# Optimization experiments

Hardware: AMD Instinct MI355X
Metric: run time of the kernel (lower is better)

## Reference

```python
import jax, jax.numpy as jnp
import numpy as np

N_TOK, D_MODEL, D_INT, N_EXP, TOP_K = 16384, 1024, 512, 8, 2


def setup_inputs() -> dict:
    key = jax.random.key(0)
    k1, k2, k3, k4 = jax.random.split(key, 4)
    x = jax.random.normal(k1, (N_TOK, D_MODEL), jnp.float32)
    # gate projection weight (n_experts, d_model)
    wg = jax.random.normal(k2, (N_EXP, D_MODEL), jnp.float32) * 0.02
    # fc1: (n_experts, 2*d_intermediate, d_model); fc2: (n_experts, d_model, d_intermediate)
    fc1 = jax.random.normal(k3, (N_EXP, 2 * D_INT, D_MODEL), jnp.float32) * (1.0 / np.sqrt(D_MODEL))
    fc2 = jax.random.normal(k4, (N_EXP, D_MODEL, D_INT), jnp.float32) * (1.0 / np.sqrt(D_INT))
    return {"x": x, "wg": wg, "fc1": fc1, "fc2": fc2, "top_k": TOP_K}


def reference(x, wg, fc1, fc2, top_k):
    # --- Gate: softmax scores, top-k selection, renormalized combine weights ---
    scores = jax.nn.softmax(x @ wg.T, axis=-1)            # (n_tok, n_exp)
    w, idx = jax.lax.top_k(scores, top_k)                 # (n_tok, k)
    w = w / jnp.sum(w, axis=-1, keepdims=True)
    # --- Routed experts: gated MLP per expert, weighted combine ---
    # Equivalent math to sort-by-expert dispatch + grouped GEMM + scatter combine:
    # each token's output = sum_k w_k * f_{idx_k}(x). We loop over the small fixed
    # expert set and mask, avoiding a (n_tok, n_exp, 2*d_int) intermediate.
    n_exp = fc1.shape[0]
    out = jnp.zeros_like(x)
    for e in range(n_exp):
        coef = jnp.sum(jnp.where(idx == e, w, 0.0), axis=-1)  # (n_tok,)
        h = x @ fc1[e].T                                      # (n_tok, 2*d_int)
        y, g = jnp.split(h, 2, axis=-1)
        y = (y * jax.nn.silu(g)) @ fc2[e].T                   # (n_tok, d_model)
        out = out + coef[:, None] * y
    return out
```

## Files before the change

### kernel.cpp

```cpp
#include <hip/hip_runtime.h>
#include <hip/hip_bf16.h>
#include <cstdint>


#define NT 16384
#define DM 1024
#define DI 512
#define NE 8
#define NB 16
#define HB 64
#define MT1 128

typedef __attribute__((ext_vector_type(8))) short bf16x8;
typedef __attribute__((ext_vector_type(4))) float f32x4;

__device__ __forceinline__ void gl16(const void* g, void* l) {
  __builtin_amdgcn_global_load_lds(
      (const __attribute__((address_space(1))) void*)g,
      (__attribute__((address_space(3))) void*)l, 16, 0, 0);
}

__device__ __forceinline__ ushort f2bf(float f) {
  uint32_t x = __float_as_uint(f);
  return (ushort)((x + 0x7fffu + ((x >> 16) & 1u)) >> 16);
}

__global__ __launch_bounds__(256) void f2bf_kernel(const float* __restrict__ in,
                                                   ushort* __restrict__ out, int n8) {
  int i = blockIdx.x * 256 + threadIdx.x;
  if (i >= n8) return;
  const float4* p = (const float4*)(in + (size_t)i * 8);
  float4 a = p[0], b = p[1];
  union { ushort u[8]; int4 v; } o;
  o.u[0] = f2bf(a.x); o.u[1] = f2bf(a.y); o.u[2] = f2bf(a.z); o.u[3] = f2bf(a.w);
  o.u[4] = f2bf(b.x); o.u[5] = f2bf(b.y); o.u[6] = f2bf(b.z); o.u[7] = f2bf(b.w);
  *(int4*)(out + (size_t)i * 8) = o.v;
}

__global__ __launch_bounds__(256) void gate_kernel(
    const float* __restrict__ x, const float* __restrict__ wg,
    int* __restrict__ topk_idx, float* __restrict__ topk_w,
    ushort* __restrict__ xb) {
  __shared__ float wgs[NE * DM];
  for (int i = threadIdx.x; i < NE * DM; i += 256) wgs[i] = wg[i];
  __syncthreads();
  const int wave = threadIdx.x >> 6;
  const int lane = threadIdx.x & 63;
  const int wid = blockIdx.x * 4 + wave;
  for (int g = 0; g < 4; ++g) {
    const int t = wid * 4 + g;
    const float* __restrict__ xr = x + (size_t)t * DM;
    ushort* __restrict__ xw = xb + (size_t)t * DM;
    float acc[NE];
#pragma unroll
    for (int e = 0; e < NE; ++e) acc[e] = 0.f;
#pragma unroll
    for (int it = 0; it < DM / 64; ++it) {
      int k = lane + it * 64;
      float xv = xr[k];
      xw[k] = f2bf(xv);
#pragma unroll
      for (int e = 0; e < NE; ++e) acc[e] += xv * wgs[e * DM + k];
    }
#pragma unroll
    for (int e = 0; e < NE; ++e) {
      float v = acc[e];
#pragma unroll
      for (int off = 32; off > 0; off >>= 1) v += __shfl_xor(v, off);
      acc[e] = v;
    }
    if (lane == 0) {
      float mx = acc[0];
#pragma unroll
      for (int e = 1; e < NE; ++e) mx = fmaxf(mx, acc[e]);
      float p[NE];
#pragma unroll
      for (int e = 0; e < NE; ++e) p[e] = __expf(acc[e] - mx);
      int i0 = 0;
#pragma unroll
      for (int e = 1; e < NE; ++e) if (p[e] > p[i0]) i0 = e;
      int i1 = -1;
#pragma unroll
      for (int e = 0; e < NE; ++e) if (e != i0 && (i1 < 0 || p[e] > p[i1])) i1 = e;
      float s = p[i0] + p[i1];
      topk_idx[t * 2 + 0] = i0;
      topk_idx[t * 2 + 1] = i1;
      topk_w[t * 2 + 0] = p[i0] / s;
      topk_w[t * 2 + 1] = p[i1] / s;
    }
  }
}

__global__ __launch_bounds__(256) void hist_kernel(const int* __restrict__ topk_idx,
                                                   int* __restrict__ blkcnt) {
  __shared__ int lc[NB];
  if (threadIdx.x < NB) lc[threadIdx.x] = 0;
  __syncthreads();
  int t = blockIdx.x * 256 + threadIdx.x;
  int e0 = topk_idx[t * 2 + 0];
  int e1 = topk_idx[t * 2 + 1];
  atomicAdd(&lc[e0], 1);
  atomicAdd(&lc[8 + e1], 1);
  __syncthreads();
  if (threadIdx.x < NB) blkcnt[blockIdx.x * NB + threadIdx.x] = lc[threadIdx.x];
}

__global__ void scan2_kernel(const int* __restrict__ blkcnt, int* __restrict__ counts,
                             int* __restrict__ offsets, int* __restrict__ blk_base) {
  __shared__ int tot[NB];
  __shared__ int offs[NB];
  const int i = threadIdx.x;
  if (i < NB) {
    int s = 0;
    for (int b = 0; b < HB; ++b) s += blkcnt[b * NB + i];
    tot[i] = s;
    counts[i] = s;
  }
  __syncthreads();
  if (i == 0) {
    int o = 0;
    for (int b = 0; b < NB; ++b) { offs[b] = o; offsets[b] = o; o += tot[b]; }
  }
  __syncthreads();
  if (i < NB) {
    int o = offs[i];
    for (int b = 0; b < HB; ++b) { blk_base[b * NB + i] = o; o += blkcnt[b * NB + i]; }
  }
}

__global__ __launch_bounds__(256) void fill_kernel(
    const int* __restrict__ topk_idx, const float* __restrict__ topk_w,
    const int* __restrict__ blk_base, int* __restrict__ bucket_tok,
    float* __restrict__ bucket_w) {
  __shared__ int lcur[NB];
  if (threadIdx.x < NB) lcur[threadIdx.x] = 0;
  __syncthreads();
  int t = blockIdx.x * 256 + threadIdx.x;
#pragma unroll
  for (int j = 0; j < 2; ++j) {
    int e = topk_idx[t * 2 + j];
    int b = j * 8 + e;
    int pos = atomicAdd(&lcur[b], 1);
    int slot = blk_base[blockIdx.x * NB + b] + pos;
    bucket_tok[slot] = t;
    bucket_w[slot] = topk_w[t * 2 + j];
  }
}

__global__ __launch_bounds__(256) void fc1_kernel(
    const ushort* __restrict__ xb, const ushort* __restrict__ fc1b,
    const int* __restrict__ counts, const int* __restrict__ offsets,
    const int* __restrict__ bucket_tok, ushort* __restrict__ z) {
  const int bid = blockIdx.x;
  const int b   = bid >> 10;
  const int rem = bid & 1023;
  const int mt  = rem >> 3;
  const int nt  = rem & 7;
  const int cnt = counts[b];
  const int m0  = mt << 7;
  if (m0 >= cnt) return;
  const int off = offsets[b];
  const int e   = b & 7;
  const int n0  = nt << 6;

  __shared__ ushort As[128 * 32];
  __shared__ ushort By[64 * 32];
  __shared__ ushort Bg[64 * 32];
  __shared__ int toks[128];

  const int t = threadIdx.x;
  if (t < 128) {
    int m = m0 + t;
    toks[t] = bucket_tok[off + ((m < cnt) ? m : (cnt - 1))];
  }
  __syncthreads();

  const int srow = t >> 2;
  const int skq  = (t & 3) * 8;
  const ushort* aG0 = xb + (size_t)toks[srow] * DM + skq;
  const ushort* aG1 = xb + (size_t)toks[64 + srow] * DM + skq;
  const ushort* fe  = fc1b + (size_t)e * (2 * DI) * DM;
  const ushort* byG = fe + (size_t)(n0 + srow) * DM + skq;
  const ushort* bgG = fe + (size_t)(DI + n0 + srow) * DM + skq;

  const int wave = t >> 6, lane = t & 63;
  const int moff = (wave >> 1) * 64;
  const int noff = (wave & 1) * 32;
  const int fr = lane & 15;
  const int fg = lane >> 4;

  f32x4 accY[4][2], accG[4][2];
#pragma unroll
  for (int i = 0; i < 4; ++i)
#pragma unroll
    for (int j = 0; j < 2; ++j) { accY[i][j] = (f32x4)0.f; accG[i][j] = (f32x4)0.f; }

  const ushort* aRd  = As + (moff + fr) * 32 + fg * 8;
  const ushort* byRd = By + (noff + fr) * 32 + fg * 8;
  const ushort* bgRd = Bg + (noff + fr) * 32 + fg * 8;
  char* AsW = (char*)As + wave * 1024;
  char* ByW = (char*)By + wave * 1024;
  char* BgW = (char*)Bg + wave * 1024;

  for (int k0 = 0; k0 < DM; k0 += 32) {
    gl16(aG0 + k0, AsW);
    gl16(aG1 + k0, AsW + 4096);
    gl16(byG + k0, ByW);
    gl16(bgG + k0, BgW);
    __syncthreads();
    bf16x8 a[4], by[2], bg[2];
#pragma unroll
    for (int i = 0; i < 4; ++i) a[i] = *(const bf16x8*)(aRd + i * 16 * 32);
#pragma unroll
    for (int j = 0; j < 2; ++j) {
      by[j] = *(const bf16x8*)(byRd + j * 16 * 32);
      bg[j] = *(const bf16x8*)(bgRd + j * 16 * 32);
    }
#pragma unroll
    for (int i = 0; i < 4; ++i)
#pragma unroll
      for (int j = 0; j < 2; ++j) {
        accY[i][j] = __builtin_amdgcn_mfma_f32_16x16x32_bf16(a[i], by[j], accY[i][j], 0, 0, 0);
        accG[i][j] = __builtin_amdgcn_mfma_f32_16x16x32_bf16(a[i], bg[j], accG[i][j], 0, 0, 0);
      }
    __syncthreads();
  }

#pragma unroll
  for (int i = 0; i < 4; ++i)
#pragma unroll
    for (int r = 0; r < 4; ++r) {
      int m = moff + i * 16 + fg * 4 + r;
      if (m0 + m < cnt) {
        ushort* zrow = z + (size_t)(off + m0 + m) * DI + n0 + noff + fr;
#pragma unroll
        for (int j = 0; j < 2; ++j) {
          float y = accY[i][j][r], g = accG[i][j][r];
          float zz = y * g / (1.f + __expf(-g));
          zrow[j * 16] = f2bf(zz);
        }
      }
    }
}

template <bool ADD>
__global__ __launch_bounds__(256) void fc2_kernel(
    const ushort* __restrict__ z, const ushort* __restrict__ fc2b,
    const int* __restrict__ counts, const int* __restrict__ offsets,
    const int* __restrict__ bucket_tok, const float* __restrict__ bucket_w,
    float* __restrict__ out, int bucket_base) {
  const int bid = blockIdx.x;
  const int b   = bucket_base + (bid >> 10);
  const int rem = bid & 1023;
  const int mt  = rem >> 3;
  const int nt  = rem & 7;
  const int cnt = counts[b];
  const int m0  = mt << 7;
  if (m0 >= cnt) return;
  const int off = offsets[b];
  const int e   = b & 7;
  const int n0  = nt << 7;

  __shared__ ushort As[128 * 32];
  __shared__ ushort Bs[128 * 32];
  __shared__ int toks[128];
  __shared__ float wts[128];

  const int t = threadIdx.x;
  if (t < 128) {
    int m = m0 + t;
    int mm = (m < cnt) ? m : (cnt - 1);
    toks[t] = bucket_tok[off + mm];
    wts[t]  = bucket_w[off + mm];
  }
  __syncthreads();

  const int srow = t >> 2;
  const int skq  = (t & 3) * 8;
  const ushort* aG = z + (size_t)(off + m0 + srow) * DI + skq;
  const ushort* bG = fc2b + (size_t)e * DM * DI + (size_t)(n0 + srow) * DI + skq;

  const int wave = t >> 6, lane = t & 63;
  const int moff = (wave >> 1) * 64;
  const int noff = (wave & 1) * 64;
  const int fr = lane & 15;
  const int fg = lane >> 4;

  f32x4 acc[4][4];
#pragma unroll
  for (int i = 0; i < 4; ++i)
#pragma unroll
    for (int j = 0; j < 4; ++j) acc[i][j] = (f32x4)0.f;

  const ushort* aRd = As + (moff + fr) * 32 + fg * 8;
  const ushort* bRd = Bs + (noff + fr) * 32 + fg * 8;
  char* AsW = (char*)As + wave * 1024;
  char* BsW = (char*)Bs + wave * 1024;

  for (int k0 = 0; k0 < DI; k0 += 32) {
    gl16(aG + k0, AsW);
    gl16(aG + (size_t)64 * DI + k0, AsW + 4096);
    gl16(bG + k0, BsW);
    gl16(bG + (size_t)64 * DI + k0, BsW + 4096);
    __syncthreads();
    bf16x8 a[4], bb[4];
#pragma unroll
    for (int i = 0; i < 4; ++i) a[i] = *(const bf16x8*)(aRd + i * 16 * 32);
#pragma unroll
    for (int j = 0; j < 4; ++j) bb[j] = *(const bf16x8*)(bRd + j * 16 * 32);
#pragma unroll
    for (int i = 0; i < 4; ++i)
#pragma unroll
      for (int j = 0; j < 4; ++j)
        acc[i][j] = __builtin_amdgcn_mfma_f32_16x16x32_bf16(a[i], bb[j], acc[i][j], 0, 0, 0);
    __syncthreads();
  }

#pragma unroll
  for (int i = 0; i < 4; ++i)
#pragma unroll
    for (int r = 0; r < 4; ++r) {
      int m = moff + i * 16 + fg * 4 + r;
      if (m0 + m < cnt) {
        int tok = toks[m];
        float w = wts[m];
        float* orow = out + (size_t)tok * DM + n0 + noff + fr;
#pragma unroll
        for (int j = 0; j < 4; ++j) {
          float v = w * acc[i][j][r];
          if (ADD) orow[j * 16] += v;
          else     orow[j * 16] = v;
        }
      }
    }
}

extern "C" void kernel_launch(void* const* d_in, const int* in_sizes, int n_in,
                              void* d_out, int out_size, void* d_ws, size_t ws_size,
                              hipStream_t stream) {
  (void)in_sizes; (void)n_in; (void)out_size; (void)ws_size;
  const float* x   = (const float*)d_in[0];
  const float* wg  = (const float*)d_in[1];
  const float* fc1 = (const float*)d_in[2];
  const float* fc2 = (const float*)d_in[3];
  float* out = (float*)d_out;

  char* p = (char*)d_ws;
  ushort* xb   = (ushort*)p; p += (size_t)NT * DM * 2;
  ushort* fc1b = (ushort*)p; p += (size_t)NE * 2 * DI * DM * 2;
  ushort* fc2b = (ushort*)p; p += (size_t)NE * DM * DI * 2;
  ushort* z    = (ushort*)p; p += ((size_t)2 * NT + 128) * DI * 2;
  int*   topk_idx   = (int*)p;   p += (size_t)NT * 2 * 4;
  float* topk_w     = (float*)p; p += (size_t)NT * 2 * 4;
  int*   bucket_tok = (int*)p;   p += (size_t)2 * NT * 4;
  float* bucket_w   = (float*)p; p += (size_t)2 * NT * 4;
  int*   counts     = (int*)p;   p += NB * 4;
  int*   offsets    = (int*)p;   p += NB * 4;
  int*   blkcnt     = (int*)p;   p += HB * NB * 4;
  int*   blk_base   = (int*)p;   p += HB * NB * 4;

  f2bf_kernel<<<(NE * 2 * DI * DM / 8 + 255) / 256, 256, 0, stream>>>(fc1, fc1b, NE * 2 * DI * DM / 8);
  f2bf_kernel<<<(NE * DM * DI / 8 + 255) / 256, 256, 0, stream>>>(fc2, fc2b, NE * DM * DI / 8);

  gate_kernel<<<1024, 256, 0, stream>>>(x, wg, topk_idx, topk_w, xb);
  hist_kernel<<<HB, 256, 0, stream>>>(topk_idx, blkcnt);
  scan2_kernel<<<1, 64, 0, stream>>>(blkcnt, counts, offsets, blk_base);
  fill_kernel<<<HB, 256, 0, stream>>>(topk_idx, topk_w, blk_base, bucket_tok, bucket_w);

  fc1_kernel<<<NB * MT1 * 8, 256, 0, stream>>>(xb, fc1b, counts, offsets, bucket_tok, z);
  fc2_kernel<false><<<8 * MT1 * 8, 256, 0, stream>>>(z, fc2b, counts, offsets,
                                                     bucket_tok, bucket_w, out, 0);
  fc2_kernel<true><<<8 * MT1 * 8, 256, 0, stream>>>(z, fc2b, counts, offsets,
                                                    bucket_tok, bucket_w, out, 8);
}
```

Baseline: 417.7 us.

## Compact tile lists for grouped GEMMs and deepen K tile with swizzled LDS

The scan kernel now builds compact lists of non-empty (bucket, m-tile) pairs, so the fc1 and fc2 launches shrink from many mostly-idle blocks to a bounded grid that maps directly onto real work. Both GEMM kernels double the K step to 64 per iteration and place tiles in LDS with an XOR swizzle to avoid bank conflicts, halving the number of barriers per GEMM. The cost is more LDS per block, which may lower occupancy, plus a serial list build on a single thread.

```diff
diff --git a/kernel.cpp b/kernel.cpp
--- a/kernel.cpp
+++ b/kernel.cpp
@@ -9,7 +9,8 @@
 #define NE 8
 #define NB 16
 #define HB 64
-#define MT1 128
+#define MAXT1 272
+#define MAXT2 136
 
 typedef __attribute__((ext_vector_type(8))) short bf16x8;
 typedef __attribute__((ext_vector_type(4))) float f32x4;
@@ -97,18 +98,17 @@
   if (threadIdx.x < NB) lc[threadIdx.x] = 0;
   __syncthreads();
   int t = blockIdx.x * 256 + threadIdx.x;
-  int e0 = topk_idx[t * 2 + 0];
-  int e1 = topk_idx[t * 2 + 1];
-  atomicAdd(&lc[e0], 1);
-  atomicAdd(&lc[8 + e1], 1);
+  atomicAdd(&lc[topk_idx[t * 2 + 0]], 1);
+  atomicAdd(&lc[8 + topk_idx[t * 2 + 1]], 1);
   __syncthreads();
   if (threadIdx.x < NB) blkcnt[blockIdx.x * NB + threadIdx.x] = lc[threadIdx.x];
 }
 
 __global__ void scan2_kernel(const int* __restrict__ blkcnt, int* __restrict__ counts,
-                             int* __restrict__ offsets, int* __restrict__ blk_base) {
-  __shared__ int tot[NB];
-  __shared__ int offs[NB];
+                             int* __restrict__ offsets, int* __restrict__ blk_base,
+                             int* __restrict__ t1_list, int* __restrict__ t2_list,
+                             int* __restrict__ nmeta) {
+  __shared__ int tot[NB], offs[NB];
   const int i = threadIdx.x;
   if (i < NB) {
     int s = 0;
@@ -125,6 +125,26 @@
   if (i < NB) {
     int o = offs[i];
     for (int b = 0; b < HB; ++b) { blk_base[b * NB + i] = o; o += blkcnt[b * NB + i]; }
+  }
+  if (i == 0) {
+    int n1 = 0;
+    for (int b = 0; b < NB; ++b) {
+      int mts = (tot[b] + 127) >> 7;
+      for (int mt = 0; mt < mts; ++mt) t1_list[n1++] = (b << 8) | mt;
+    }
+    nmeta[0] = n1;
+    int n2 = 0;
+    for (int b = 0; b < 8; ++b) {
+      int mts = (tot[b] + 127) >> 7;
+      for (int mt = 0; mt < mts; ++mt) t2_list[n2++] = (b << 8) | mt;
+    }
+    nmeta[1] = n2;
+    int n3 = 0;
+    for (int b = 8; b < NB; ++b) {
+      int mts = (tot[b] + 127) >> 7;
+      for (int mt = 0; mt < mts; ++mt) t2_list[MAXT2 + n3++] = (b << 8) | mt;
+    }
+    nmeta[2] = n3;
   }
 }
 
@@ -150,22 +170,19 @@
 __global__ __launch_bounds__(256) void fc1_kernel(
     const ushort* __restrict__ xb, const ushort* __restrict__ fc1b,
     const int* __restrict__ counts, const int* __restrict__ offsets,
-    const int* __restrict__ bucket_tok, ushort* __restrict__ z) {
-  const int bid = blockIdx.x;
-  const int b   = bid >> 10;
-  const int rem = bid & 1023;
-  const int mt  = rem >> 3;
-  const int nt  = rem & 7;
-  const int cnt = counts[b];
-  const int m0  = mt << 7;
-  if (m0 >= cnt) return;
-  const int off = offsets[b];
-  const int e   = b & 7;
-  const int n0  = nt << 6;
-
-  __shared__ ushort As[128 * 32];
-  __shared__ ushort By[64 * 32];
-  __shared__ ushort Bg[64 * 32];
+    const int* __restrict__ bucket_tok, const int* __restrict__ t1_list,
+    const int* __restrict__ nmeta, ushort* __restrict__ z) {
+  const int tl = blockIdx.x >> 3;
+  if (tl >= nmeta[0]) return;
+  const int nt = blockIdx.x & 7;
+  const int d = t1_list[tl];
+  const int b = d >> 8, mt = d & 255;
+  const int cnt = counts[b], off = offsets[b], e = b & 7;
+  const int m0 = mt << 7, n0 = nt << 6;
+
+  __shared__ ushort As[128 * 64];
+  __shared__ ushort By[64 * 64];
+  __shared__ ushort Bg[64 * 64];
   __shared__ int toks[128];
 
   const int t = threadIdx.x;
@@ -175,54 +192,76 @@
   }
   __syncthreads();
 
-  const int srow = t >> 2;
-  const int skq  = (t & 3) * 8;
-  const ushort* aG0 = xb + (size_t)toks[srow] * DM + skq;
-  const ushort* aG1 = xb + (size_t)toks[64 + srow] * DM + skq;
-  const ushort* fe  = fc1b + (size_t)e * (2 * DI) * DM;
-  const ushort* byG = fe + (size_t)(n0 + srow) * DM + skq;
-  const ushort* bgG = fe + (size_t)(DI + n0 + srow) * DM + skq;
-
+  const int rA = t >> 3;
+  const int g8 = (((t & 7) ^ (rA & 7)) << 3);
   const int wave = t >> 6, lane = t & 63;
-  const int moff = (wave >> 1) * 64;
-  const int noff = (wave & 1) * 32;
-  const int fr = lane & 15;
-  const int fg = lane >> 4;
-
-  f32x4 accY[4][2], accG[4][2];
-#pragma unroll
-  for (int i = 0; i < 4; ++i)
-#pragma unroll
-    for (int j = 0; j < 2; ++j) { accY[i][j] = (f32x4)0.f; accG[i][j] = (f32x4)0.f; }
-
-  const ushort* aRd  = As + (moff + fr) * 32 + fg * 8;
-  const ushort* byRd = By + (noff + fr) * 32 + fg * 8;
-  const ushort* bgRd = Bg + (noff + fr) * 32 + fg * 8;
+
+  const ushort* aSrc0 = xb + (size_t)toks[rA] * DM + g8;
+  const ushort* aSrc1 = xb + (size_t)toks[32 + rA] * DM + g8;
+  const ushort* aSrc2 = xb + (size_t)toks[64 + rA] * DM + g8;
+  const ushort* aSrc3 = xb + (size_t)toks[96 + rA] * DM + g8;
+  const ushort* fe = fc1b + (size_t)e * (2 * DI) * DM;
+  const ushort* ySrc0 = fe + (size_t)(n0 + rA) * DM + g8;
+  const ushort* ySrc1 = fe + (size_t)(n0 + 32 + rA) * DM + g8;
+  const ushort* gSrc0 = fe + (size_t)(DI + n0 + rA) * DM + g8;
+  const ushort* gSrc1 = fe + (size_t)(DI + n0 + 32 + rA) * DM + g8;
+
   char* AsW = (char*)As + wave * 1024;
   char* ByW = (char*)By + wave * 1024;
   char* BgW = (char*)Bg + wave * 1024;
 
-  for (int k0 = 0; k0 < DM; k0 += 32) {
-    gl16(aG0 + k0, AsW);
-    gl16(aG1 + k0, AsW + 4096);
-    gl16(byG + k0, ByW);
-    gl16(bgG + k0, BgW);
+  const int moff = (wave >> 1) * 64, noff = (wave & 1) * 32;
+  const int fr = lane & 15, fg = lane >> 4;
+  const int c0 = ((fg ^ (fr & 7)) << 4);
+  const int c1 = (((4 + fg) ^ (fr & 7)) << 4);
+  const char* aRd = (const char*)As + (moff + fr) * 128;
+  const char* yRd = (const char*)By + (noff + fr) * 128;
+  const char* gRd = (const char*)Bg + (noff + fr) * 128;
+
+  f32x4 accY[4][2], accG[4][2];
+#pragma unroll
+  for (int i = 0; i < 4; ++i)
+#pragma unroll
+    for (int j = 0; j < 2; ++j) { accY[i][j] = (f32x4)0.f; accG[i][j] = (f32x4)0.f; }
+
+  for (int k0 = 0; k0 < DM; k0 += 64) {
+    gl16(aSrc0 + k0, AsW);
+    gl16(aSrc1 + k0, AsW + 4096);
+    gl16(aSrc2 + k0, AsW + 8192);
+    gl16(aSrc3 + k0, AsW + 12288);
+    gl16(ySrc0 + k0, ByW);
+    gl16(ySrc1 + k0, ByW + 4096);
+    gl16(gSrc0 + k0, BgW);
+    gl16(gSrc1 + k0, BgW + 4096);
     __syncthreads();
-    bf16x8 a[4], by[2], bg[2];
-#pragma unroll
-    for (int i = 0; i < 4; ++i) a[i] = *(const bf16x8*)(aRd + i * 16 * 32);
-#pragma unroll
-    for (int j = 0; j < 2; ++j) {
-      by[j] = *(const bf16x8*)(byRd + j * 16 * 32);
-      bg[j] = *(const bf16x8*)(bgRd + j * 16 * 32);
-    }
-#pragma unroll
-    for (int i = 0; i < 4; ++i)
-#pragma unroll
-      for (int j = 0; j < 2; ++j) {
-        accY[i][j] = __builtin_amdgcn_mfma_f32_16x16x32_bf16(a[i], by[j], accY[i][j], 0, 0, 0);
-        accG[i][j] = __builtin_amdgcn_mfma_f32_16x16x32_bf16(a[i], bg[j], accG[i][j], 0, 0, 0);
-      }
+#pragma unroll
+    for (int ks = 0; ks < 2; ++ks) {
+      const int cc = ks ? c1 : c0;
+      bf16x8 a0 = *(const bf16x8*)(aRd + 0 * 2048 + cc);
+      bf16x8 a1 = *(const bf16x8*)(aRd + 1 * 2048 + cc);
+      bf16x8 a2 = *(const bf16x8*)(aRd + 2 * 2048 + cc);
+      bf16x8 a3 = *(const bf16x8*)(aRd + 3 * 2048 + cc);
+      bf16x8 y0 = *(const bf16x8*)(yRd + 0 * 2048 + cc);
+      bf16x8 y1 = *(const bf16x8*)(yRd + 1 * 2048 + cc);
+      bf16x8 g0 = *(const bf16x8*)(gRd + 0 * 2048 + cc);
+      bf16x8 g1 = *(const bf16x8*)(gRd + 1 * 2048 + cc);
+      accY[0][0] = __builtin_amdgcn_mfma_f32_16x16x32_bf16(a0, y0, accY[0][0], 0, 0, 0);
+      accY[1][0] = __builtin_amdgcn_mfma_f32_16x16x32_bf16(a1, y0, accY[1][0], 0, 0, 0);
+      accY[2][0] = __builtin_amdgcn_mfma_f32_16x16x32_bf16(a2, y0, accY[2][0], 0, 0, 0);
+      accY[3][0] = __builtin_amdgcn_mfma_f32_16x16x32_bf16(a3, y0, accY[3][0], 0, 0, 0);
+      accY[0][1] = __builtin_amdgcn_mfma_f32_16x16x32_bf16(a0, y1, accY[0][1], 0, 0, 0);
+      accY[1][1] = __builtin_amdgcn_mfma_f32_16x16x32_bf16(a1, y1, accY[1][1], 0, 0, 0);
+      accY[2][1] = __builtin_amdgcn_mfma_f32_16x16x32_bf16(a2, y1, accY[2][1], 0, 0, 0);
+      accY[3][1] = __builtin_amdgcn_mfma_f32_16x16x32_bf16(a3, y1, accY[3][1], 0, 0, 0);
+      accG[0][0] = __builtin_amdgcn_mfma_f32_16x16x32_bf16(a0, g0, accG[0][0], 0, 0, 0);
+      accG[1][0] = __builtin_amdgcn_mfma_f32_16x16x32_bf16(a1, g0, accG[1][0], 0, 0, 0);
+      accG[2][0] = __builtin_amdgcn_mfma_f32_16x16x32_bf16(a2, g0, accG[2][0], 0, 0, 0);
+      accG[3][0] = __builtin_amdgcn_mfma_f32_16x16x32_bf16(a3, g0, accG[3][0], 0, 0, 0);
+      accG[0][1] = __builtin_amdgcn_mfma_f32_16x16x32_bf16(a0, g1, accG[0][1], 0, 0, 0);
+      accG[1][1] = __builtin_amdgcn_mfma_f32_16x16x32_bf16(a1, g1, accG[1][1], 0, 0, 0);
+      accG[2][1] = __builtin_amdgcn_mfma_f32_16x16x32_bf16(a2, g1, accG[2][1], 0, 0, 0);
+      accG[3][1] = __builtin_amdgcn_mfma_f32_16x16x32_bf16(a3, g1, accG[3][1], 0, 0, 0);
+    }
     __syncthreads();
   }
 
@@ -248,21 +287,18 @@
     const ushort* __restrict__ z, const ushort* __restrict__ fc2b,
     const int* __restrict__ counts, const int* __restrict__ offsets,
     const int* __restrict__ bucket_tok, const float* __restrict__ bucket_w,
-    float* __restrict__ out, int bucket_base) {
-  const int bid = blockIdx.x;
-  const int b   = bucket_base + (bid >> 10);
-  const int rem = bid & 1023;
-  const int mt  = rem >> 3;
-  const int nt  = rem & 7;
-  const int cnt = counts[b];
-  const int m0  = mt << 7;
-  if (m0 >= cnt) return;
-  const int off = offsets[b];
-  const int e   = b & 7;
-  const int n0  = nt << 7;
-
-  __shared__ ushort As[128 * 32];
-  __shared__ ushort Bs[128 * 32];
+    const int* __restrict__ t2_list, const int* __restrict__ nmeta,
+    float* __restrict__ out) {
+  const int tl = blockIdx.x >> 3;
+  if (tl >= nmeta[ADD ? 2 : 1]) return;
+  const int nt = blockIdx.x & 7;
+  const int d = t2_list[(ADD ? MAXT2 : 0) + tl];
+  const int b = d >> 8, mt = d & 255;
+  const int cnt = counts[b], off = offsets[b], e = b & 7;
+  const int m0 = mt << 7, n0 = nt << 7;
+
+  __shared__ ushort As[128 * 64];
+  __shared__ ushort Bs[128 * 64];
   __shared__ int toks[128];
   __shared__ float wts[128];
 
@@ -271,48 +307,64 @@
     int m = m0 + t;
     int mm = (m < cnt) ? m : (cnt - 1);
     toks[t] = bucket_tok[off + mm];
-    wts[t]  = bucket_w[off + mm];
-  }
-  __syncthreads();
-
-  const int srow = t >> 2;
-  const int skq  = (t & 3) * 8;
-  const ushort* aG = z + (size_t)(off + m0 + srow) * DI + skq;
-  const ushort* bG = fc2b + (size_t)e * DM * DI + (size_t)(n0 + srow) * DI + skq;
-
+    wts[t] = bucket_w[off + mm];
+  }
+  __syncthreads();
+
+  const int rA = t >> 3;
+  const int g8 = (((t & 7) ^ (rA & 7)) << 3);
   const int wave = t >> 6, lane = t & 63;
-  const int moff = (wave >> 1) * 64;
-  const int noff = (wave & 1) * 64;
-  const int fr = lane & 15;
-  const int fg = lane >> 4;
-
-  f32x4 acc[4][4];
-#pragma unroll
-  for (int i = 0; i < 4; ++i)
-#pragma unroll
-    for (int j = 0; j < 4; ++j) acc[i][j] = (f32x4)0.f;
-
-  const ushort* aRd = As + (moff + fr) * 32 + fg * 8;
-  const ushort* bRd = Bs + (noff + fr) * 32 + fg * 8;
+
+  const ushort* aSrc0 = z + (size_t)(off + m0 + rA) * DI + g8;
+  const ushort* fb = fc2b + (size_t)e * DM * DI;
+  const ushort* bSrc0 = fb + (size_t)(n0 + rA) * DI + g8;
+
   char* AsW = (char*)As + wave * 1024;
   char* BsW = (char*)Bs + wave * 1024;
 
-  for (int k0 = 0; k0 < DI; k0 += 32) {
-    gl16(aG + k0, AsW);
-    gl16(aG + (size_t)64 * DI + k0, AsW + 4096);
-    gl16(bG + k0, BsW);
-    gl16(bG + (size_t)64 * DI + k0, BsW + 4096);
+  const int moff = (wave >> 1) * 64, noff = (wave & 1) * 64;
+  const int fr = lane & 15, fg = lane >> 4;
+  const int c0 = ((fg ^ (fr & 7)) << 4);
+  const int c1 = (((4 + fg) ^ (fr & 7)) << 4);
+  const char* aRd = (const char*)As + (moff + fr) * 128;
+  const char* bRd = (const char*)Bs + (noff + fr) * 128;
+
+  f32x4 acc[4][4];
+#pragma unroll
+  for (int i = 0; i < 4; ++i)
+#pragma unroll
+    for (int j = 0; j < 4; ++j) acc[i][j] = (f32x4)0.f;
+
+  for (int k0 = 0; k0 < DI; k0 += 64) {
+    gl16(aSrc0 + k0, AsW);
+    gl16(aSrc0 + (size_t)32 * DI + k0, AsW + 4096);
+    gl16(aSrc0 + (size_t)64 * DI + k0, AsW + 8192);
+    gl16(aSrc0 + (size_t)96 * DI + k0, AsW + 12288);
+    gl16(bSrc0 + k0, BsW);
+    gl16(bSrc0 + (size_t)32 * DI + k0, BsW + 4096);
+    gl16(bSrc0 + (size_t)64 * DI + k0, BsW + 8192);
+    gl16(bSrc0 + (size_t)96 * DI + k0, BsW + 12288);
     __syncthreads();
-    bf16x8 a[4], bb[4];
-#pragma unroll
-    for (int i = 0; i < 4; ++i) a[i] = *(const bf16x8*)(aRd + i * 16 * 32);
-#pragma unroll
-    for (int j = 0; j < 4; ++j) bb[j] = *(const bf16x8*)(bRd + j * 16 * 32);
-#pragma unroll
-    for (int i = 0; i < 4; ++i)
-#pragma unroll
-      for (int j = 0; j < 4; ++j)
-        acc[i][j] = __builtin_amdgcn_mfma_f32_16x16x32_bf16(a[i], bb[j], acc[i][j], 0, 0, 0);
+#pragma unroll
+    for (int ks = 0; ks < 2; ++ks) {
+      const int cc = ks ? c1 : c0;
+      bf16x8 a0 = *(const bf16x8*)(aRd + 0 * 2048 + cc);
+      bf16x8 a1 = *(const bf16x8*)(aRd + 1 * 2048 + cc);
+      bf16x8 a2 = *(const bf16x8*)(aRd + 2 * 2048 + cc);
+      bf16x8 a3 = *(const bf16x8*)(aRd + 3 * 2048 + cc);
+      bf16x8 b0 = *(const bf16x8*)(bRd + 0 * 2048 + cc);
+      bf16x8 b1 = *(const bf16x8*)(bRd + 1 * 2048 + cc);
+      bf16x8 b2 = *(const bf16x8*)(bRd + 2 * 2048 + cc);
+      bf16x8 b3 = *(const bf16x8*)(bRd + 3 * 2048 + cc);
+#pragma unroll
+      for (int i = 0; i < 4; ++i) {
+        bf16x8 ai = (i == 0) ? a0 : (i == 1) ? a1 : (i == 2) ? a2 : a3;
+        acc[i][0] = __builtin_amdgcn_mfma_f32_16x16x32_bf16(ai, b0, acc[i][0], 0, 0, 0);
+        acc[i][1] = __builtin_amdgcn_mfma_f32_16x16x32_bf16(ai, b1, acc[i][1], 0, 0, 0);
+        acc[i][2] = __builtin_amdgcn_mfma_f32_16x16x32_bf16(ai, b2, acc[i][2], 0, 0, 0);
+        acc[i][3] = __builtin_amdgcn_mfma_f32_16x16x32_bf16(ai, b3, acc[i][3], 0, 0, 0);
+      }
+    }
     __syncthreads();
   }
 
@@ -358,18 +410,22 @@
   int*   offsets    = (int*)p;   p += NB * 4;
   int*   blkcnt     = (int*)p;   p += HB * NB * 4;
   int*   blk_base   = (int*)p;   p += HB * NB * 4;
+  int*   t1_list    = (int*)p;   p += MAXT1 * 4;
+  int*   t2_list    = (int*)p;   p += 2 * MAXT2 * 4;
+  int*   nmeta      = (int*)p;   p += 4 * 4;
 
   f2bf_kernel<<<(NE * 2 * DI * DM / 8 + 255) / 256, 256, 0, stream>>>(fc1, fc1b, NE * 2 * DI * DM / 8);
   f2bf_kernel<<<(NE * DM * DI / 8 + 255) / 256, 256, 0, stream>>>(fc2, fc2b, NE * DM * DI / 8);
 
   gate_kernel<<<1024, 256, 0, stream>>>(x, wg, topk_idx, topk_w, xb);
   hist_kernel<<<HB, 256, 0, stream>>>(topk_idx, blkcnt);
-  scan2_kernel<<<1, 64, 0, stream>>>(blkcnt, counts, offsets, blk_base);
+  scan2_kernel<<<1, 64, 0, stream>>>(blkcnt, counts, offsets, blk_base, t1_list, t2_list, nmeta);
   fill_kernel<<<HB, 256, 0, stream>>>(topk_idx, topk_w, blk_base, bucket_tok, bucket_w);
 
-  fc1_kernel<<<NB * MT1 * 8, 256, 0, stream>>>(xb, fc1b, counts, offsets, bucket_tok, z);
-  fc2_kernel<false><<<8 * MT1 * 8, 256, 0, stream>>>(z, fc2b, counts, offsets,
-                                                     bucket_tok, bucket_w, out, 0);
-  fc2_kernel<true><<<8 * MT1 * 8, 256, 0, stream>>>(z, fc2b, counts, offsets,
-                                                    bucket_tok, bucket_w, out, 8);
-}
+  fc1_kernel<<<MAXT1 * 8, 256, 0, stream>>>(xb, fc1b, counts, offsets, bucket_tok,
+                                            t1_list, nmeta, z);
+  fc2_kernel<false><<<MAXT2 * 8, 256, 0, stream>>>(z, fc2b, counts, offsets, bucket_tok,
+                                                   bucket_w, t2_list, nmeta, out);
+  fc2_kernel<true><<<MAXT2 * 8, 256, 0, stream>>>(z, fc2b, counts, offsets, bucket_tok,
+                                                  bucket_w, t2_list, nmeta, out);
+}
```

Result: slower. 428.2 us (+2.5%).
